# Kernel tuning notes

Measured on AMD Instinct MI355X. Metric: run time of the kernel, lower is better.

## Reference

```python
import jax, jax.numpy as jnp
import numpy as np

N, E, D, L = 50000, 800000, 96, 4
IN_H, IN_E, HID, OUT = 26, 4, 128, 8
BN_EPS, AGG_EPS = 1e-5, 1e-6


def setup_inputs() -> dict:
    key = jax.random.key(0)
    ks = jax.random.split(key, 24)
    f32 = jnp.float32
    nrm = lambda k, sh, s=0.05: jax.random.normal(k, sh, f32) * s
    inp = {
        "h1": nrm(ks[0], (N, 6), 1.0),
        "h2": nrm(ks[1], (N, 4), 1.0),
        "z": nrm(ks[2], (N, 16), 1.0),
        "efeat": nrm(ks[3], (E, IN_E), 1.0),
        "max_action": jnp.ones((N, 1), f32),
        "Wh_emb": nrm(ks[4], (IN_H, D)), "bh_emb": jnp.zeros((D,), f32),
        "We_emb": nrm(ks[5], (IN_E, D)), "be_emb": jnp.zeros((D,), f32),
        "WA": nrm(ks[6], (L, D, D)), "bA": jnp.zeros((L, D), f32),
        "WB": nrm(ks[7], (L, D, D)), "bB": jnp.zeros((L, D), f32),
        "WC": nrm(ks[8], (L, D, D)), "bC": jnp.zeros((L, D), f32),
        "WD": nrm(ks[9], (L, D, D)), "bD": jnp.zeros((L, D), f32),
        "WE": nrm(ks[10], (L, D, D)), "bE": jnp.zeros((L, D), f32),
        "bn_h_g": jnp.ones((L, D), f32), "bn_h_b": jnp.zeros((L, D), f32),
        "bn_e_g": jnp.ones((L, D), f32), "bn_e_b": jnp.zeros((L, D), f32),
        "W1": nrm(ks[11], (D, HID)), "b1": jnp.zeros((HID,), f32),
        "W2": nrm(ks[12], (HID, OUT)), "b2": jnp.zeros((OUT,), f32),
        "src": jax.random.randint(ks[13], (E,), 0, N),
        "dst": jax.random.randint(ks[14], (E,), 0, N),
    }
    return inp


def _bn(x, g, b):
    # BatchNorm1d in train mode: batch stats over node/edge axis, biased var
    mu = x.mean(axis=0)
    var = x.var(axis=0)
    return g * (x - mu) * jax.lax.rsqrt(var + BN_EPS) + b


def reference(h1, h2, z, efeat, max_action, Wh_emb, bh_emb, We_emb, be_emb,
              WA, bA, WB, bB, WC, bC, WD, bD, WE, bE,
              bn_h_g, bn_h_b, bn_e_g, bn_e_b, W1, b1, W2, b2, src, dst):
    # input embedding  (Actor concat: states then z)
    h = jnp.concatenate([h1, h2, z], axis=-1) @ Wh_emb + bh_emb   # [N, D]
    e = efeat @ We_emb + be_emb                                    # [E, D]
    n = h.shape[0]
    for l in range(L):  # GatedGCN layers (residual + BN + ReLU)
        Ah = h @ WA[l] + bA[l]
        Bh = h @ WB[l] + bB[l]
        Dh = h @ WD[l] + bD[l]
        Eh = h @ WE[l] + bE[l]
        Ce = e @ WC[l] + bC[l]
        e_new = Dh[src] + Eh[dst] + Ce                             # [E, D]
        sig = jax.nn.sigmoid(e_new)
        num = jax.ops.segment_sum(sig * Bh[src], dst, num_segments=n)
        den = jax.ops.segment_sum(sig, dst, num_segments=n)
        h_new = Ah + num / (den + AGG_EPS)
        h = h + jax.nn.relu(_bn(h_new, bn_h_g[l], bn_h_b[l]))
        e = e + jax.nn.relu(_bn(e_new, bn_e_g[l], bn_e_b[l]))
    # MLP head + tanh scale
    out = jax.nn.relu(h @ W1 + b1) @ W2 + b2                        # [N, OUT]
    return max_action * jnp.tanh(out)
```

## Files before the change

### kernel.cpp

```cpp
#include <hip/hip_runtime.h>
#include <math.h>

#define NN 50000
#define EE 800000
#define DD 96
#define NHID 128
#define NOUT 8
#define LDA 104

typedef unsigned int uint32;
typedef float floatx2 __attribute__((ext_vector_type(2)));
typedef float f32x4 __attribute__((ext_vector_type(4)));
typedef short bf16x8 __attribute__((ext_vector_type(8)));

__device__ __forceinline__ float bfu2f(ushort u) {
  union { uint32 u; float f; } v; v.u = ((uint32)u) << 16; return v.f;
}
__device__ __forceinline__ ushort f2bf(float x) {
  union { float f; uint32 u; } v; v.f = x;
  uint32 r = (v.u + 0x7fffu + ((v.u >> 16) & 1u)) >> 16;
  return (ushort)r;
}

template <int ESZ> struct EST;
template <> struct EST<2> {
  typedef ushort4 Raw;
  static __device__ __forceinline__ Raw ldraw(const void* e, size_t grp) {
    return ((const ushort4*)e)[grp];
  }
  static __device__ __forceinline__ float4 dec(Raw a) {
    return make_float4(bfu2f(a.x), bfu2f(a.y), bfu2f(a.z), bfu2f(a.w));
  }
  static __device__ __forceinline__ float4 ld(const void* e, size_t grp) {
    return dec(ldraw(e, grp));
  }
  static __device__ __forceinline__ void st(void* e, size_t grp, float4 v) {
    ushort4 o; o.x = f2bf(v.x); o.y = f2bf(v.y); o.z = f2bf(v.z); o.w = f2bf(v.w);
    ((ushort4*)e)[grp] = o;
  }
  static __device__ __forceinline__ float ld1c(const void* e, size_t pos, int c) {
    return bfu2f(((const ushort*)e)[pos * DD + c]);
  }
};
template <> struct EST<1> {
  typedef int Raw;
  static __device__ __forceinline__ Raw ldraw(const void* e, size_t grp) {
    return ((const int*)e)[grp];
  }
  static __device__ __forceinline__ float4 dec(Raw u) {
    floatx2 lo = __builtin_amdgcn_cvt_pk_f32_fp8(u, false);
    floatx2 hi = __builtin_amdgcn_cvt_pk_f32_fp8(u, true);
    return make_float4(lo[0], lo[1], hi[0], hi[1]);
  }
  static __device__ __forceinline__ float4 ld(const void* e, size_t grp) {
    return dec(ldraw(e, grp));
  }
  static __device__ __forceinline__ void st(void* e, size_t grp, float4 v) {
    int u = 0;
    u = __builtin_amdgcn_cvt_pk_fp8_f32(v.x, v.y, u, false);
    u = __builtin_amdgcn_cvt_pk_fp8_f32(v.z, v.w, u, true);
    ((int*)e)[grp] = u;
  }
  static __device__ __forceinline__ float ld1c(const void* e, size_t pos, int c) {
    const int dw = ((const int*)e)[pos * (DD / 4) + (c >> 2)];
    floatx2 lo = __builtin_amdgcn_cvt_pk_f32_fp8(dw, false);
    floatx2 hi = __builtin_amdgcn_cvt_pk_f32_fp8(dw, true);
    return (c & 2) ? ((c & 1) ? hi[1] : hi[0]) : ((c & 1) ? lo[1] : lo[0]);
  }
};

__global__ __launch_bounds__(256) void k_zero_init(int* __restrict__ cnt,
    float* __restrict__ stats) {
  int i = blockIdx.x * 256 + threadIdx.x;
  const int str = gridDim.x * 256;
  for (; i < NN; i += str) cnt[i] = 0;
  if (blockIdx.x == 0)
    for (int j = threadIdx.x; j < 768; j += 256) stats[j] = 0.f;
}

__global__ __launch_bounds__(256) void k_hist(const int* __restrict__ dst,
    int* __restrict__ cnt) {
  const int i = blockIdx.x * 256 + threadIdx.x;
  if (i < EE) atomicAdd(&cnt[dst[i]], 1);
}

__global__ __launch_bounds__(256) void k_scan(const int* __restrict__ cnt,
    int* __restrict__ rowptr, int* __restrict__ cursor) {
  __shared__ int part[256];
  const int t = threadIdx.x;
  const int CH = (NN + 255) / 256;
  const int lo = t * CH, hi = min((t + 1) * CH, NN);
  int s = 0;
  for (int i = lo; i < hi; i++) s += cnt[i];
  part[t] = s;
  __syncthreads();
  for (int off = 1; off < 256; off <<= 1) {
    int v = (t >= off) ? part[t - off] : 0;
    __syncthreads();
    part[t] += v;
    __syncthreads();
  }
  int base = (t == 0) ? 0 : part[t - 1];
  for (int i = lo; i < hi; i++) {
    rowptr[i] = base; cursor[i] = base; base += cnt[i];
  }
  if (t == 255) rowptr[NN] = base;
}

__global__ __launch_bounds__(256) void k_scatter(const int* __restrict__ src,
    const int* __restrict__ dst, int* __restrict__ cursor,
    int* __restrict__ perm, int* __restrict__ srcC, int* __restrict__ dstC) {
  const int i = blockIdx.x * 256 + threadIdx.x;
  if (i < EE) {
    const int d = dst[i];
    const int pos = atomicAdd(&cursor[d], 1);
    perm[pos] = i; srcC[pos] = src[i]; dstC[pos] = d;
  }
}

__global__ __launch_bounds__(256) void k_embed_h(const float* __restrict__ h1,
    const float* __restrict__ h2, const float* __restrict__ z,
    const float* __restrict__ W, const float* __restrict__ b,
    ushort* __restrict__ h) {
  int idx = blockIdx.x * 256 + threadIdx.x;
  const int total = NN * DD;
  const int stride = gridDim.x * 256;
  for (; idx < total; idx += stride) {
    int n = idx / DD, c = idx - n * DD;
    float acc = b[c];
#pragma unroll
    for (int k = 0; k < 6; k++)  acc = fmaf(h1[n * 6 + k], W[k * DD + c], acc);
#pragma unroll
    for (int k = 0; k < 4; k++)  acc = fmaf(h2[n * 4 + k], W[(6 + k) * DD + c], acc);
#pragma unroll
    for (int k = 0; k < 16; k++) acc = fmaf(z[n * 16 + k], W[(10 + k) * DD + c], acc);
    h[idx] = f2bf(acc);
  }
}

template <int EZ>
__global__ __launch_bounds__(256) void k_embed_e(const float* __restrict__ ef,
    const float* __restrict__ W, const float* __restrict__ b,
    const int* __restrict__ perm, void* __restrict__ e) {
  int g = blockIdx.x * 256 + threadIdx.x;
  const int totalg = EE * (DD / 4);
  const int stride = gridDim.x * 256;
  for (; g < totalg; g += stride) {
    const int pos = g / 24, cg = (g - pos * 24) * 4;
    const int orig = perm[pos];
    const float f0 = ef[orig * 4], f1 = ef[orig * 4 + 1];
    const float f2 = ef[orig * 4 + 2], f3 = ef[orig * 4 + 3];
    float4 acc;
    acc.x = b[cg+0] + f0*W[cg+0] + f1*W[DD+cg+0] + f2*W[2*DD+cg+0] + f3*W[3*DD+cg+0];
    acc.y = b[cg+1] + f0*W[cg+1] + f1*W[DD+cg+1] + f2*W[2*DD+cg+1] + f3*W[3*DD+cg+1];
    acc.z = b[cg+2] + f0*W[cg+2] + f1*W[DD+cg+2] + f2*W[2*DD+cg+2] + f3*W[3*DD+cg+2];
    acc.w = b[cg+3] + f0*W[cg+3] + f1*W[DD+cg+3] + f2*W[2*DD+cg+3] + f3*W[3*DD+cg+3];
    EST<EZ>::st(e, g, acc);
  }
}

template <int LAZY>
__global__ __launch_bounds__(256) void k_ngemm(ushort* __restrict__ h,
    const float* __restrict__ WAp, const float* __restrict__ WBp,
    const float* __restrict__ WDp, const float* __restrict__ WEp,
    const float* __restrict__ bAp, const float* __restrict__ bBp,
    const float* __restrict__ bDp, const float* __restrict__ bEp,
    ushort* __restrict__ oA, ushort* __restrict__ oB,
    ushort* __restrict__ oD, ushort* __restrict__ oE,
    const float* __restrict__ stats) {
  __shared__ __align__(16) ushort Wt[DD * LDA];
  __shared__ __align__(16) ushort At[128 * LDA];
  __shared__ float uscl[DD], ushf[DD];
  const int tid = threadIdx.x;
  if (LAZY && tid < DD) { uscl[tid] = stats[384 + tid]; ushf[tid] = stats[480 + tid]; }
  if (LAZY) __syncthreads();
  const int base = blockIdx.x * 128;
#pragma unroll
  for (int ii = 0; ii < 12; ii++) {
    const int i = ii * 256 + tid;
    const int r = i / 24, q = i - (i / 24) * 24;
    const int row = base + r;
    ushort4 a; a.x = 0; a.y = 0; a.z = 0; a.w = 0;
    if (row < NN) a = ((const ushort4*)h)[(size_t)row * 24 + q];
    if (LAZY && row < NN) {
      const ushort4 u = ((const ushort4*)oA)[(size_t)row * 24 + q];
      const int c = q * 4;
      float f0 = bfu2f(a.x) + fmaxf(fmaf(bfu2f(u.x), uscl[c],     ushf[c]),     0.f);
      float f1 = bfu2f(a.y) + fmaxf(fmaf(bfu2f(u.y), uscl[c + 1], ushf[c + 1]), 0.f);
      float f2 = bfu2f(a.z) + fmaxf(fmaf(bfu2f(u.z), uscl[c + 2], ushf[c + 2]), 0.f);
      float f3 = bfu2f(a.w) + fmaxf(fmaf(bfu2f(u.w), uscl[c + 3], ushf[c + 3]), 0.f);
      a.x = f2bf(f0); a.y = f2bf(f1); a.z = f2bf(f2); a.w = f2bf(f3);
      ((ushort4*)h)[(size_t)row * 24 + q] = a;
    }
    *(ushort4*)&At[r * LDA + q * 4] = a;
  }
  const int w = tid >> 6, lane = tid & 63;
  const int lrow = lane & 15, lgrp = lane >> 4;
#pragma unroll
  for (int m = 0; m < 4; m++) {
    const float* W  = (m == 0) ? WAp : (m == 1) ? WBp : (m == 2) ? WDp : WEp;
    const float* bi = (m == 0) ? bAp : (m == 1) ? bBp : (m == 2) ? bDp : bEp;
    ushort* out     = (m == 0) ? oA  : (m == 1) ? oB  : (m == 2) ? oD  : oE;
#pragma unroll
    for (int ii = 0; ii < 36; ii++) {
      const int i = ii * 256 + tid;
      const int k = i / DD, n = i - (i / DD) * DD;
      Wt[n * LDA + k] = f2bf(W[i]);
    }
    __syncthreads();
    f32x4 acc[2][6];
#pragma unroll
    for (int rt2 = 0; rt2 < 2; rt2++)
#pragma unroll
      for (int nt = 0; nt < 6; nt++) {
        acc[rt2][nt][0] = 0.f; acc[rt2][nt][1] = 0.f;
        acc[rt2][nt][2] = 0.f; acc[rt2][nt][3] = 0.f;
      }
#pragma unroll
    for (int rt2 = 0; rt2 < 2; rt2++) {
      const int rt = w * 2 + rt2;
#pragma unroll
      for (int kk = 0; kk < 3; kk++) {
        const bf16x8 af = *(const bf16x8*)&At[(rt * 16 + lrow) * LDA + kk * 32 + lgrp * 8];
#pragma unroll
        for (int nt = 0; nt < 6; nt++) {
          const bf16x8 bfr = *(const bf16x8*)&Wt[(nt * 16 + lrow) * LDA + kk * 32 + lgrp * 8];
          acc[rt2][nt] = __builtin_amdgcn_mfma_f32_16x16x32_bf16(af, bfr, acc[rt2][nt], 0, 0, 0);
        }
      }
    }
#pragma unroll
    for (int rt2 = 0; rt2 < 2; rt2++) {
      const int rt = w * 2 + rt2;
#pragma unroll
      for (int j = 0; j < 4; j++) {
        const int row = base + rt * 16 + lgrp * 4 + j;
        if (row < NN) {
#pragma unroll
          for (int nt = 0; nt < 6; nt++) {
            const int ch = nt * 16 + lrow;
            out[(size_t)row * DD + ch] = f2bf(acc[rt2][nt][j] + bi[ch]);
          }
        }
      }
    }
    __syncthreads();
  }
}

template <int MODE, int EZE, int EZN>
__global__ __launch_bounds__(256) void k_edge(void* __restrict__ e,
    void* __restrict__ e_new,
    const float* __restrict__ WC, const float* __restrict__ bC,
    const ushort* __restrict__ Dh, const ushort* __restrict__ Eh,
    const int* __restrict__ srcC, const int* __restrict__ dstC,
    float* __restrict__ stats) {
  __shared__ __align__(16) ushort Wt[DD * LDA];
  __shared__ __align__(16) ushort At[64 * LDA];
  __shared__ float sred[2 * DD];
  __shared__ float escl[DD], eshl[DD];
  __shared__ int sidx_s[64], sidx_d[64];
  const int tid = threadIdx.x;
  for (int i = tid; i < DD * DD; i += 256) {
    const int k = i / DD, n = i - (i / DD) * DD;
    Wt[n * LDA + k] = f2bf(WC[i]);
  }
  if (tid < 2 * DD) sred[tid] = 0.f;
  if (MODE >= 1 && tid < DD) { escl[tid] = stats[576 + tid]; eshl[tid] = stats[672 + tid]; }
  __syncthreads();
  const int w = tid >> 6, lane = tid & 63;
  const int lrow = lane & 15, lgrp = lane >> 4;
  const int qq0 = lane % 24;
  const int qq1 = (lane + 16) % 24;
  const int qq2 = (lane + 8) % 24;
  const float4 bc0 = *(const float4*)&bC[qq0 * 4];
  const float4 bc1 = *(const float4*)&bC[qq1 * 4];
  const float4 bc2 = *(const float4*)&bC[qq2 * 4];
  float sacc0[4] = {0,0,0,0}, sacc1[4] = {0,0,0,0}, sacc2[4] = {0,0,0,0};
  float qacc0[4] = {0,0,0,0}, qacc1[4] = {0,0,0,0}, qacc2[4] = {0,0,0,0};

  const int NT = EE / 64;
  typename EST<EZE>::Raw pe[6];
  typename EST<EZN>::Raw pn[6];
  int ps = 0, pd = 0;
  {
    const size_t b24 = (size_t)blockIdx.x * 64 * 24;
#pragma unroll
    for (int ii = 0; ii < 6; ii++) {
      const int i = ii * 256 + tid;
      pe[ii] = EST<EZE>::ldraw(e, b24 + i);
      if (MODE >= 1) pn[ii] = EST<EZN>::ldraw(e_new, b24 + i);
    }
    if (tid < 64) {
      ps = srcC[blockIdx.x * 64 + tid];
      pd = dstC[blockIdx.x * 64 + tid];
    }
  }
  for (int t = blockIdx.x; t < NT; t += gridDim.x) {
    const size_t base = (size_t)t * 64;
    const size_t b24 = base * 24;
#pragma unroll
    for (int ii = 0; ii < 6; ii++) {
      const int i = ii * 256 + tid;
      const int r = i / 24, gq = i - (i / 24) * 24;
      float4 a = EST<EZE>::dec(pe[ii]);
      if (MODE >= 1) {
        const float4 d = EST<EZN>::dec(pn[ii]);
        const int c = gq * 4;
        a.x += fmaxf(fmaf(d.x, escl[c],     eshl[c]),     0.f);
        a.y += fmaxf(fmaf(d.y, escl[c + 1], eshl[c + 1]), 0.f);
        a.z += fmaxf(fmaf(d.z, escl[c + 2], eshl[c + 2]), 0.f);
        a.w += fmaxf(fmaf(d.w, escl[c + 3], eshl[c + 3]), 0.f);
        if (MODE == 1) EST<EZE>::st(e, b24 + i, a);
      }
      ushort4 o; o.x = f2bf(a.x); o.y = f2bf(a.y); o.z = f2bf(a.z); o.w = f2bf(a.w);
      *(ushort4*)&At[r * LDA + gq * 4] = o;
    }
    if (tid < 64) { sidx_s[tid] = ps; sidx_d[tid] = pd; }
    const int tn = t + gridDim.x;
    if (tn < NT) {
      const size_t bn = (size_t)tn * 64 * 24;
#pragma unroll
      for (int ii = 0; ii < 6; ii++) {
        const int i = ii * 256 + tid;
        pe[ii] = EST<EZE>::ldraw(e, bn + i);
        if (MODE >= 1) pn[ii] = EST<EZN>::ldraw(e_new, bn + i);
      }
      if (tid < 64) { ps = srcC[tn * 64 + tid]; pd = dstC[tn * 64 + tid]; }
    }
    __syncthreads();
    f32x4 acc[6];
#pragma unroll
    for (int nt = 0; nt < 6; nt++) { acc[nt][0]=0.f; acc[nt][1]=0.f; acc[nt][2]=0.f; acc[nt][3]=0.f; }
#pragma unroll
    for (int kk = 0; kk < 3; kk++) {
      const bf16x8 af = *(const bf16x8*)&At[(w * 16 + lrow) * LDA + kk * 32 + lgrp * 8];
#pragma unroll
      for (int nt = 0; nt < 6; nt++) {
        const bf16x8 bfr = *(const bf16x8*)&Wt[(nt * 16 + lrow) * LDA + kk * 32 + lgrp * 8];
        acc[nt] = __builtin_amdgcn_mfma_f32_16x16x32_bf16(af, bfr, acc[nt], 0, 0, 0);
      }
    }
#pragma unroll
    for (int j = 0; j < 4; j++) {
#pragma unroll
      for (int nt = 0; nt < 6; nt++) {
        At[(w * 16 + lgrp * 4 + j) * LDA + nt * 16 + lrow] = f2bf(acc[nt][j]);
      }
    }
#pragma unroll
    for (int it = 0; it < 6; it++) {
      const int idx = it * 64 + lane;
      const int r16 = idx / 24, gq = idx - (idx / 24) * 24;
      const int row = w * 16 + r16;
      const size_t pos = base + row;
      const int s = sidx_s[row], d2 = sidx_d[row];
      const ushort4 av = *(const ushort4*)&At[row * LDA + gq * 4];
      const ushort4 dv = *(const ushort4*)&Dh[(size_t)s * DD + gq * 4];
      const ushort4 ev = *(const ushort4*)&Eh[(size_t)d2 * DD + gq * 4];
      const float4 bc = (it % 3 == 0) ? bc0 : (it % 3 == 1) ? bc1 : bc2;
      float4 v;
      v.x = bfu2f(av.x) + bc.x + bfu2f(dv.x) + bfu2f(ev.x);
      v.y = bfu2f(av.y) + bc.y + bfu2f(dv.y) + bfu2f(ev.y);
      v.z = bfu2f(av.z) + bc.z + bfu2f(dv.z) + bfu2f(ev.z);
      v.w = bfu2f(av.w) + bc.w + bfu2f(dv.w) + bfu2f(ev.w);
      if (it % 3 == 0) {
        sacc0[0]+=v.x; sacc0[1]+=v.y; sacc0[2]+=v.z; sacc0[3]+=v.w;
        qacc0[0]+=v.x*v.x; qacc0[1]+=v.y*v.y; qacc0[2]+=v.z*v.z; qacc0[3]+=v.w*v.w;
      } else if (it % 3 == 1) {
        sacc1[0]+=v.x; sacc1[1]+=v.y; sacc1[2]+=v.z; sacc1[3]+=v.w;
        qacc1[0]+=v.x*v.x; qacc1[1]+=v.y*v.y; qacc1[2]+=v.z*v.z; qacc1[3]+=v.w*v.w;
      } else {
        sacc2[0]+=v.x; sacc2[1]+=v.y; sacc2[2]+=v.z; sacc2[3]+=v.w;
        qacc2[0]+=v.x*v.x; qacc2[1]+=v.y*v.y; qacc2[2]+=v.z*v.z; qacc2[3]+=v.w*v.w;
      }
      EST<EZN>::st(e_new, pos * 24 + gq, v);
    }
    __syncthreads();
  }
#pragma unroll
  for (int c = 0; c < 4; c++) {
    atomicAdd(&sred[qq0 * 4 + c], sacc0[c]);
    atomicAdd(&sred[DD + qq0 * 4 + c], qacc0[c]);
    atomicAdd(&sred[qq1 * 4 + c], sacc1[c]);
    atomicAdd(&sred[DD + qq1 * 4 + c], qacc1[c]);
    atomicAdd(&sred[qq2 * 4 + c], sacc2[c]);
    atomicAdd(&sred[DD + qq2 * 4 + c], qacc2[c]);
  }
  __syncthreads();
  if (tid < 2 * DD) atomicAdd(&stats[tid], sred[tid]);
}

template <int EZN>
__global__ __launch_bounds__(256) void k_agg(const void* __restrict__ e_new,
    const int* __restrict__ srcC, const int* __restrict__ rowptr,
    const ushort* __restrict__ Bh, ushort* __restrict__ hn,
    float* __restrict__ stats) {
  __shared__ float sred[2 * DD];
  if (threadIdx.x < 2 * DD) sred[threadIdx.x] = 0.f;
  __syncthreads();
  const int hw = threadIdx.x >> 5, lane = threadIdx.x & 31;
  const int c0 = lane, c1 = lane + 32, c2 = lane + 64;
  float sa0 = 0, sa1 = 0, sa2 = 0, qa0 = 0, qa1 = 0, qa2 = 0;
  for (int n = blockIdx.x * 8 + hw; n < NN; n += gridDim.x * 8) {
    const int rs = rowptr[n], re = rowptr[n + 1];
    float n0 = 0, n1 = 0, n2 = 0, d0 = 0, d1 = 0, d2 = 0;
    int p = rs;
    for (; p + 2 <= re; p += 2) {
      const int sA = srcC[p], sB = srcC[p + 1];
      const float vA0 = EST<EZN>::ld1c(e_new, (size_t)p, c0);
      const float vA1 = EST<EZN>::ld1c(e_new, (size_t)p, c1);
      const float vA2 = EST<EZN>::ld1c(e_new, (size_t)p, c2);
      const float vB0 = EST<EZN>::ld1c(e_new, (size_t)(p + 1), c0);
      const float vB1 = EST<EZN>::ld1c(e_new, (size_t)(p + 1), c1);
      const float vB2 = EST<EZN>::ld1c(e_new, (size_t)(p + 1), c2);
      const size_t sbA = (size_t)sA * DD, sbB = (size_t)sB * DD;
      const float bA0 = bfu2f(Bh[sbA + c0]), bA1 = bfu2f(Bh[sbA + c1]), bA2 = bfu2f(Bh[sbA + c2]);
      const float bB0 = bfu2f(Bh[sbB + c0]), bB1 = bfu2f(Bh[sbB + c1]), bB2 = bfu2f(Bh[sbB + c2]);
      const float gA0 = 1.f / (1.f + __expf(-vA0));
      const float gA1 = 1.f / (1.f + __expf(-vA1));
      const float gA2 = 1.f / (1.f + __expf(-vA2));
      const float gB0 = 1.f / (1.f + __expf(-vB0));
      const float gB1 = 1.f / (1.f + __expf(-vB1));
      const float gB2 = 1.f / (1.f + __expf(-vB2));
      n0 += gA0 * bA0 + gB0 * bB0; d0 += gA0 + gB0;
      n1 += gA1 * bA1 + gB1 * bB1; d1 += gA1 + gB1;
      n2 += gA2 * bA2 + gB2 * bB2; d2 += gA2 + gB2;
    }
    if (p < re) {
      const int s = srcC[p];
      const float v0 = EST<EZN>::ld1c(e_new, (size_t)p, c0);
      const float v1 = EST<EZN>::ld1c(e_new, (size_t)p, c1);
      const float v2 = EST<EZN>::ld1c(e_new, (size_t)p, c2);
      const float g0 = 1.f / (1.f + __expf(-v0));
      const float g1 = 1.f / (1.f + __expf(-v1));
      const float g2 = 1.f / (1.f + __expf(-v2));
      const size_t sb = (size_t)s * DD;
      n0 += g0 * bfu2f(Bh[sb + c0]); d0 += g0;
      n1 += g1 * bfu2f(Bh[sb + c1]); d1 += g1;
      n2 += g2 * bfu2f(Bh[sb + c2]); d2 += g2;
    }
    const size_t hb = (size_t)n * DD;
    const float v0 = bfu2f(hn[hb + c0]) + n0 / (d0 + 1e-6f);
    const float v1 = bfu2f(hn[hb + c1]) + n1 / (d1 + 1e-6f);
    const float v2 = bfu2f(hn[hb + c2]) + n2 / (d2 + 1e-6f);
    hn[hb + c0] = f2bf(v0); hn[hb + c1] = f2bf(v1); hn[hb + c2] = f2bf(v2);
    sa0 += v0; qa0 += v0 * v0;
    sa1 += v1; qa1 += v1 * v1;
    sa2 += v2; qa2 += v2 * v2;
  }
  atomicAdd(&sred[c0], sa0); atomicAdd(&sred[c1], sa1); atomicAdd(&sred[c2], sa2);
  atomicAdd(&sred[DD + c0], qa0); atomicAdd(&sred[DD + c1], qa1); atomicAdd(&sred[DD + c2], qa2);
  __syncthreads();
  if (threadIdx.x < 2 * DD) atomicAdd(&stats[192 + threadIdx.x], sred[threadIdx.x]);
}

__global__ void k_finalize(float* __restrict__ stats,
    const float* __restrict__ g_h, const float* __restrict__ b_h,
    const float* __restrict__ g_e, const float* __restrict__ b_e) {
  const int c = threadIdx.x;
  if (c < DD) {
    const float mu_h = stats[192 + c] / (float)NN;
    const float var_h = stats[288 + c] / (float)NN - mu_h * mu_h;
    const float sc_h = g_h[c] * rsqrtf(var_h + 1e-5f);
    const float mu_e = stats[c] / (float)EE;
    const float var_e = stats[96 + c] / (float)EE - mu_e * mu_e;
    const float sc_e = g_e[c] * rsqrtf(var_e + 1e-5f);
    stats[384 + c] = sc_h;
    stats[480 + c] = b_h[c] - mu_h * sc_h;
    stats[576 + c] = sc_e;
    stats[672 + c] = b_e[c] - mu_e * sc_e;
    stats[c] = 0.f; stats[96 + c] = 0.f; stats[192 + c] = 0.f; stats[288 + c] = 0.f;
  }
}

__global__ __launch_bounds__(256) void k_head(const ushort* __restrict__ h,
    const ushort* __restrict__ hn, const float* __restrict__ stats,
    const float* __restrict__ W1, const float* __restrict__ b1,
    const float* __restrict__ W2, const float* __restrict__ b2,
    const float* __restrict__ ma, float* __restrict__ out) {
  __shared__ float W1l[DD * NHID];
  __shared__ float W2l[NHID * NOUT];
  __shared__ float hid[4][NHID];
  __shared__ float hrow[4][DD];
  __shared__ float uscl[DD], ushf[DD];
  for (int i = threadIdx.x; i < DD * NHID; i += 256) W1l[i] = W1[i];
  for (int i = threadIdx.x; i < NHID * NOUT; i += 256) W2l[i] = W2[i];
  if (threadIdx.x < DD) {
    uscl[threadIdx.x] = stats[384 + threadIdx.x];
    ushf[threadIdx.x] = stats[480 + threadIdx.x];
  }
  __syncthreads();
  const int w = threadIdx.x >> 6, lane = threadIdx.x & 63;
  for (int n = blockIdx.x * 4 + w; n < NN; n += gridDim.x * 4) {
    const ushort* hp = h + (size_t)n * DD;
    const ushort* up = hn + (size_t)n * DD;
    hrow[w][lane] = bfu2f(hp[lane])
        + fmaxf(fmaf(bfu2f(up[lane]), uscl[lane], ushf[lane]), 0.f);
    if (lane < DD - 64)
      hrow[w][64 + lane] = bfu2f(hp[64 + lane])
          + fmaxf(fmaf(bfu2f(up[64 + lane]), uscl[64 + lane], ushf[64 + lane]), 0.f);
    float a0 = b1[lane], a1 = b1[64 + lane];
    for (int k = 0; k < DD; k++) {
      const float x = hrow[w][k];
      a0 = fmaf(x, W1l[k * NHID + lane], a0);
      a1 = fmaf(x, W1l[k * NHID + 64 + lane], a1);
    }
    hid[w][lane] = fmaxf(a0, 0.f);
    hid[w][64 + lane] = fmaxf(a1, 0.f);
    if (lane < NOUT) {
      float o = b2[lane];
      for (int k = 0; k < NHID; k++) o = fmaf(hid[w][k], W2l[k * NOUT + lane], o);
      out[(size_t)n * NOUT + lane] = ma[n] * tanhf(o);
    }
  }
}

extern "C" void kernel_launch(void* const* d_in, const int* in_sizes, int n_in,
                              void* d_out, int out_size, void* d_ws, size_t ws_size,
                              hipStream_t stream) {
  const float* h1  = (const float*)d_in[0];
  const float* h2  = (const float*)d_in[1];
  const float* z   = (const float*)d_in[2];
  const float* ef  = (const float*)d_in[3];
  const float* ma  = (const float*)d_in[4];
  const float* Wh  = (const float*)d_in[5];
  const float* bh  = (const float*)d_in[6];
  const float* We  = (const float*)d_in[7];
  const float* be  = (const float*)d_in[8];
  const float* WA  = (const float*)d_in[9];
  const float* bA  = (const float*)d_in[10];
  const float* WB  = (const float*)d_in[11];
  const float* bB  = (const float*)d_in[12];
  const float* WC  = (const float*)d_in[13];
  const float* bC  = (const float*)d_in[14];
  const float* WD  = (const float*)d_in[15];
  const float* bD  = (const float*)d_in[16];
  const float* WE  = (const float*)d_in[17];
  const float* bE  = (const float*)d_in[18];
  const float* bn_h_g = (const float*)d_in[19];
  const float* bn_h_b = (const float*)d_in[20];
  const float* bn_e_g = (const float*)d_in[21];
  const float* bn_e_b = (const float*)d_in[22];
  const float* W1  = (const float*)d_in[23];
  const float* b1  = (const float*)d_in[24];
  const float* W2  = (const float*)d_in[25];
  const float* b2  = (const float*)d_in[26];
  const int*   src = (const int*)d_in[27];
  const int*   dst = (const int*)d_in[28];

  const size_t E_ELEMS = (size_t)EE * DD;
  const size_t N_ELEMS = (size_t)NN * DD;
  int tier;
  if (ws_size >= 455000000UL)      tier = 0;
  else if (ws_size >= 297000000UL) tier = 1;
  else                             tier = 2;
  const size_t esze = (tier == 0) ? 2 : 1;
  const size_t eszn = (tier <= 1) ? 2 : 1;

  char* p = (char*)d_ws;
  void* e     = (void*)p; p += E_ELEMS * esze;
  void* e_new = (void*)p; p += E_ELEMS * eszn;
  ushort* h   = (ushort*)p; p += N_ELEMS * 2;
  ushort* hn  = (ushort*)p; p += N_ELEMS * 2;
  ushort* Bhb = (ushort*)p; p += N_ELEMS * 2;
  ushort* Dhb = (ushort*)p; p += N_ELEMS * 2;
  ushort* Ehb = (ushort*)p; p += N_ELEMS * 2;
  int* cnt    = (int*)p; p += (size_t)NN * 4;
  int* rowptr = (int*)p; p += (size_t)(NN + 1) * 4;
  int* cursor = (int*)p; p += (size_t)NN * 4;
  int* perm   = (int*)p; p += (size_t)EE * 4;
  int* srcC   = (int*)p; p += (size_t)EE * 4;
  int* dstC   = (int*)p; p += (size_t)EE * 4;
  float* stats = (float*)p;

  k_zero_init<<<64, 256, 0, stream>>>(cnt, stats);
  k_hist<<<3125, 256, 0, stream>>>(dst, cnt);
  k_scan<<<1, 256, 0, stream>>>(cnt, rowptr, cursor);
  k_scatter<<<3125, 256, 0, stream>>>(src, dst, cursor, perm, srcC, dstC);
  k_embed_h<<<1024, 256, 0, stream>>>(h1, h2, z, Wh, bh, h);
  if (esze == 2) k_embed_e<2><<<2048, 256, 0, stream>>>(ef, We, be, perm, e);
  else           k_embed_e<1><<<2048, 256, 0, stream>>>(ef, We, be, perm, e);

  for (int l = 0; l < 4; l++) {
#define NG_ARGS h, WA + l*DD*DD, WB + l*DD*DD, WD + l*DD*DD, WE + l*DD*DD, \
    bA + l*DD, bB + l*DD, bD + l*DD, bE + l*DD, hn, Bhb, Dhb, Ehb, stats
    if (l == 0) k_ngemm<0><<<391, 256, 0, stream>>>(NG_ARGS);
    else        k_ngemm<1><<<391, 256, 0, stream>>>(NG_ARGS);
#undef NG_ARGS
    const float* WCl = WC + l * DD * DD;
    const float* bCl = bC + l * DD;
#define EDGE_ARGS e, e_new, WCl, bCl, Dhb, Ehb, srcC, dstC, stats
    if (tier == 0) {
      if (l == 0)      k_edge<0,2,2><<<1250, 256, 0, stream>>>(EDGE_ARGS);
      else if (l < 3)  k_edge<1,2,2><<<1250, 256, 0, stream>>>(EDGE_ARGS);
      else             k_edge<2,2,2><<<1250, 256, 0, stream>>>(EDGE_ARGS);
    } else if (tier == 1) {
      if (l == 0)      k_edge<0,1,2><<<1250, 256, 0, stream>>>(EDGE_ARGS);
      else if (l < 3)  k_edge<1,1,2><<<1250, 256, 0, stream>>>(EDGE_ARGS);
      else             k_edge<2,1,2><<<1250, 256, 0, stream>>>(EDGE_ARGS);
    } else {
      if (l == 0)      k_edge<0,1,1><<<1250, 256, 0, stream>>>(EDGE_ARGS);
      else if (l < 3)  k_edge<1,1,1><<<1250, 256, 0, stream>>>(EDGE_ARGS);
      else             k_edge<2,1,1><<<1250, 256, 0, stream>>>(EDGE_ARGS);
    }
#undef EDGE_ARGS
    if (eszn == 2) k_agg<2><<<1024, 256, 0, stream>>>(e_new, srcC, rowptr, Bhb, hn, stats);
    else           k_agg<1><<<1024, 256, 0, stream>>>(e_new, srcC, rowptr, Bhb, hn, stats);
    k_finalize<<<1, 128, 0, stream>>>(stats,
        bn_h_g + l * DD, bn_h_b + l * DD, bn_e_g + l * DD, bn_e_b + l * DD);
  }

  k_head<<<1024, 256, 0, stream>>>(h, hn, stats, W1, b1, W2, b2, ma, (float*)d_out);
}
```

Before: 1.856 ms.

## Pre-convert weights to transposed bf16 once, unroll aggregation by four, double agg grid

A new prep kernel converts all per-layer node and edge weight matrices to bf16 in transposed layout once. The ngemm and edge kernels then load them into LDS with vectorized ushort4 copies instead of strided fp32 loads and per-element conversion in every block. The aggregation loop is unrolled to four edges so more gathers are in flight, and its grid is doubled. The extra weight buffer in the workspace required nudging the tier threshold, and the prep launch adds a small fixed cost.

```diff
diff --git a/kernel.cpp b/kernel.cpp
--- a/kernel.cpp
+++ b/kernel.cpp
@@ -76,6 +76,21 @@
   for (; i < NN; i += str) cnt[i] = 0;
   if (blockIdx.x == 0)
     for (int j = threadIdx.x; j < 768; j += 256) stats[j] = 0.f;
+}
+
+__global__ __launch_bounds__(256) void k_prep(const float* __restrict__ WA,
+    const float* __restrict__ WB, const float* __restrict__ WD,
+    const float* __restrict__ WE, const float* __restrict__ WC,
+    ushort* __restrict__ Wbf) {
+  int gid = blockIdx.x * 256 + threadIdx.x;
+  const int total = 20 * DD * DD;
+  for (; gid < total; gid += gridDim.x * 256) {
+    const int m = gid / (DD * DD), rem = gid - m * (DD * DD);
+    const int n = rem / DD, k = rem - (rem / DD) * DD;
+    const int l = m / 5, j = m - (m / 5) * 5;
+    const float* src = (j == 0) ? WA : (j == 1) ? WB : (j == 2) ? WD : (j == 3) ? WE : WC;
+    Wbf[gid] = f2bf(src[l * DD * DD + k * DD + n]);
+  }
 }
 
 __global__ __launch_bounds__(256) void k_hist(const int* __restrict__ dst,
@@ -161,8 +176,7 @@
 
 template <int LAZY>
 __global__ __launch_bounds__(256) void k_ngemm(ushort* __restrict__ h,
-    const float* __restrict__ WAp, const float* __restrict__ WBp,
-    const float* __restrict__ WDp, const float* __restrict__ WEp,
+    const ushort* __restrict__ Wbf5,
     const float* __restrict__ bAp, const float* __restrict__ bBp,
     const float* __restrict__ bDp, const float* __restrict__ bEp,
     ushort* __restrict__ oA, ushort* __restrict__ oB,
@@ -198,14 +212,14 @@
   const int lrow = lane & 15, lgrp = lane >> 4;
 #pragma unroll
   for (int m = 0; m < 4; m++) {
-    const float* W  = (m == 0) ? WAp : (m == 1) ? WBp : (m == 2) ? WDp : WEp;
     const float* bi = (m == 0) ? bAp : (m == 1) ? bBp : (m == 2) ? bDp : bEp;
     ushort* out     = (m == 0) ? oA  : (m == 1) ? oB  : (m == 2) ? oD  : oE;
-#pragma unroll
-    for (int ii = 0; ii < 36; ii++) {
-      const int i = ii * 256 + tid;
-      const int k = i / DD, n = i - (i / DD) * DD;
-      Wt[n * LDA + k] = f2bf(W[i]);
+    const ushort* Wm = Wbf5 + m * (DD * DD);
+#pragma unroll
+    for (int ii = 0; ii < 9; ii++) {
+      const int i4 = ii * 256 + tid;
+      const int n = i4 / 24, k4 = i4 - (i4 / 24) * 24;
+      *(ushort4*)&Wt[n * LDA + k4 * 4] = ((const ushort4*)Wm)[i4];
     }
     __syncthreads();
     f32x4 acc[2][6];
@@ -251,7 +265,7 @@
 template <int MODE, int EZE, int EZN>
 __global__ __launch_bounds__(256) void k_edge(void* __restrict__ e,
     void* __restrict__ e_new,
-    const float* __restrict__ WC, const float* __restrict__ bC,
+    const ushort* __restrict__ WCbf, const float* __restrict__ bC,
     const ushort* __restrict__ Dh, const ushort* __restrict__ Eh,
     const int* __restrict__ srcC, const int* __restrict__ dstC,
     float* __restrict__ stats) {
@@ -261,9 +275,11 @@
   __shared__ float escl[DD], eshl[DD];
   __shared__ int sidx_s[64], sidx_d[64];
   const int tid = threadIdx.x;
-  for (int i = tid; i < DD * DD; i += 256) {
-    const int k = i / DD, n = i - (i / DD) * DD;
-    Wt[n * LDA + k] = f2bf(WC[i]);
+#pragma unroll
+  for (int ii = 0; ii < 9; ii++) {
+    const int i4 = ii * 256 + tid;
+    const int n = i4 / 24, k4 = i4 - (i4 / 24) * 24;
+    *(ushort4*)&Wt[n * LDA + k4 * 4] = ((const ushort4*)WCbf)[i4];
   }
   if (tid < 2 * DD) sred[tid] = 0.f;
   if (MODE >= 1 && tid < DD) { escl[tid] = stats[576 + tid]; eshl[tid] = stats[672 + tid]; }
@@ -406,28 +422,30 @@
     const int rs = rowptr[n], re = rowptr[n + 1];
     float n0 = 0, n1 = 0, n2 = 0, d0 = 0, d1 = 0, d2 = 0;
     int p = rs;
-    for (; p + 2 <= re; p += 2) {
-      const int sA = srcC[p], sB = srcC[p + 1];
-      const float vA0 = EST<EZN>::ld1c(e_new, (size_t)p, c0);
-      const float vA1 = EST<EZN>::ld1c(e_new, (size_t)p, c1);
-      const float vA2 = EST<EZN>::ld1c(e_new, (size_t)p, c2);
-      const float vB0 = EST<EZN>::ld1c(e_new, (size_t)(p + 1), c0);
-      const float vB1 = EST<EZN>::ld1c(e_new, (size_t)(p + 1), c1);
-      const float vB2 = EST<EZN>::ld1c(e_new, (size_t)(p + 1), c2);
-      const size_t sbA = (size_t)sA * DD, sbB = (size_t)sB * DD;
-      const float bA0 = bfu2f(Bh[sbA + c0]), bA1 = bfu2f(Bh[sbA + c1]), bA2 = bfu2f(Bh[sbA + c2]);
-      const float bB0 = bfu2f(Bh[sbB + c0]), bB1 = bfu2f(Bh[sbB + c1]), bB2 = bfu2f(Bh[sbB + c2]);
-      const float gA0 = 1.f / (1.f + __expf(-vA0));
-      const float gA1 = 1.f / (1.f + __expf(-vA1));
-      const float gA2 = 1.f / (1.f + __expf(-vA2));
-      const float gB0 = 1.f / (1.f + __expf(-vB0));
-      const float gB1 = 1.f / (1.f + __expf(-vB1));
-      const float gB2 = 1.f / (1.f + __expf(-vB2));
-      n0 += gA0 * bA0 + gB0 * bB0; d0 += gA0 + gB0;
-      n1 += gA1 * bA1 + gB1 * bB1; d1 += gA1 + gB1;
-      n2 += gA2 * bA2 + gB2 * bB2; d2 += gA2 + gB2;
-    }
-    if (p < re) {
+    for (; p + 4 <= re; p += 4) {
+      float v0[4], v1[4], v2[4], b0[4], b1[4], b2[4];
+#pragma unroll
+      for (int j = 0; j < 4; j++) {
+        const int s = srcC[p + j];
+        v0[j] = EST<EZN>::ld1c(e_new, (size_t)(p + j), c0);
+        v1[j] = EST<EZN>::ld1c(e_new, (size_t)(p + j), c1);
+        v2[j] = EST<EZN>::ld1c(e_new, (size_t)(p + j), c2);
+        const size_t sb = (size_t)s * DD;
+        b0[j] = bfu2f(Bh[sb + c0]);
+        b1[j] = bfu2f(Bh[sb + c1]);
+        b2[j] = bfu2f(Bh[sb + c2]);
+      }
+#pragma unroll
+      for (int j = 0; j < 4; j++) {
+        const float g0 = 1.f / (1.f + __expf(-v0[j]));
+        const float g1 = 1.f / (1.f + __expf(-v1[j]));
+        const float g2 = 1.f / (1.f + __expf(-v2[j]));
+        n0 += g0 * b0[j]; d0 += g0;
+        n1 += g1 * b1[j]; d1 += g1;
+        n2 += g2 * b2[j]; d2 += g2;
+      }
+    }
+    for (; p < re; p++) {
       const int s = srcC[p];
       const float v0 = EST<EZN>::ld1c(e_new, (size_t)p, c0);
       const float v1 = EST<EZN>::ld1c(e_new, (size_t)p, c1);
@@ -553,7 +571,7 @@
   const size_t N_ELEMS = (size_t)NN * DD;
   int tier;
   if (ws_size >= 455000000UL)      tier = 0;
-  else if (ws_size >= 297000000UL) tier = 1;
+  else if (ws_size >= 298000000UL) tier = 1;
   else                             tier = 2;
   const size_t esze = (tier == 0) ? 2 : 1;
   const size_t eszn = (tier <= 1) ? 2 : 1;
@@ -572,9 +590,11 @@
   int* perm   = (int*)p; p += (size_t)EE * 4;
   int* srcC   = (int*)p; p += (size_t)EE * 4;
   int* dstC   = (int*)p; p += (size_t)EE * 4;
+  ushort* Wbf = (ushort*)p; p += (size_t)20 * DD * DD * 2;
   float* stats = (float*)p;
 
   k_zero_init<<<64, 256, 0, stream>>>(cnt, stats);
+  k_prep<<<720, 256, 0, stream>>>(WA, WB, WD, WE, WC, Wbf);
   k_hist<<<3125, 256, 0, stream>>>(dst, cnt);
   k_scan<<<1, 256, 0, stream>>>(cnt, rowptr, cursor);
   k_scatter<<<3125, 256, 0, stream>>>(src, dst, cursor, perm, srcC, dstC);
@@ -583,14 +603,15 @@
   else           k_embed_e<1><<<2048, 256, 0, stream>>>(ef, We, be, perm, e);
 
   for (int l = 0; l < 4; l++) {
-#define NG_ARGS h, WA + l*DD*DD, WB + l*DD*DD, WD + l*DD*DD, WE + l*DD*DD, \
-    bA + l*DD, bB + l*DD, bD + l*DD, bE + l*DD, hn, Bhb, Dhb, Ehb, stats
+    const ushort* Wbf5 = Wbf + (size_t)l * 5 * DD * DD;
+#define NG_ARGS h, Wbf5, bA + l*DD, bB + l*DD, bD + l*DD, bE + l*DD, \
+    hn, Bhb, Dhb, Ehb, stats
     if (l == 0) k_ngemm<0><<<391, 256, 0, stream>>>(NG_ARGS);
     else        k_ngemm<1><<<391, 256, 0, stream>>>(NG_ARGS);
 #undef NG_ARGS
-    const float* WCl = WC + l * DD * DD;
+    const ushort* WCbf = Wbf5 + 4 * DD * DD;
     const float* bCl = bC + l * DD;
-#define EDGE_ARGS e, e_new, WCl, bCl, Dhb, Ehb, srcC, dstC, stats
+#define EDGE_ARGS e, e_new, WCbf, bCl, Dhb, Ehb, srcC, dstC, stats
     if (tier == 0) {
       if (l == 0)      k_edge<0,2,2><<<1250, 256, 0, stream>>>(EDGE_ARGS);
       else if (l < 3)  k_edge<1,2,2><<<1250, 256, 0, stream>>>(EDGE_ARGS);
@@ -605,8 +626,8 @@
       else             k_edge<2,1,1><<<1250, 256, 0, stream>>>(EDGE_ARGS);
     }
 #undef EDGE_ARGS
-    if (eszn == 2) k_agg<2><<<1024, 256, 0, stream>>>(e_new, srcC, rowptr, Bhb, hn, stats);
-    else           k_agg<1><<<1024, 256, 0, stream>>>(e_new, srcC, rowptr, Bhb, hn, stats);
+    if (eszn == 2) k_agg<2><<<2048, 256, 0, stream>>>(e_new, srcC, rowptr, Bhb, hn, stats);
+    else           k_agg<1><<<2048, 256, 0, stream>>>(e_new, srcC, rowptr, Bhb, hn, stats);
     k_finalize<<<1, 128, 0, stream>>>(stats,
         bn_h_g + l * DD, bn_h_b + l * DD, bn_e_g + l * DD, bn_e_b + l * DD);
   }
```

New measurement: 1.850 ms. Within noise of the previous version (-0.3%).
